# Kernel tuning notes

Measured on AMD Instinct MI355X. Metric: run time of the kernel, lower is better.

## Reference

```python
import jax, jax.numpy as jnp
import numpy as np
from jax import lax


def _l2norm(x):
    return x / jnp.sqrt(jnp.sum(x * x, axis=-1, keepdims=True) + 1e-6)


def setup_inputs() -> dict:
    key = jax.random.key(0)
    kq, kk, kv, kb = jax.random.split(key, 4)
    b, h, L, d = 2, 8, 4096, 128
    return {
        "q": jax.random.normal(kq, (b, h, L, d), dtype=jnp.float32),
        "k": jax.random.normal(kk, (b, h, L, d), dtype=jnp.float32),
        "v": jax.random.normal(kv, (b, h, L, d), dtype=jnp.float32),
        "beta": jax.random.uniform(kb, (b, h, L), dtype=jnp.float32),
        "chunk_size": 32,
    }


def reference(q, k, v, beta, chunk_size):
    # Chunk-wise Delta-rule linear attention (faithful to delta_rule_chunkwise).
    b, h, L, dk = q.shape
    dv = v.shape[-1]
    c = int(chunk_size)
    pad = (-L) % c
    if pad:
        q = jnp.pad(q, ((0, 0), (0, 0), (0, pad), (0, 0)))
        k = jnp.pad(k, ((0, 0), (0, 0), (0, pad), (0, 0)))
        v = jnp.pad(v, ((0, 0), (0, 0), (0, pad), (0, 0)))
        beta = jnp.pad(beta, ((0, 0), (0, 0), (0, pad)))
    Lp = L + pad
    n = Lp // c

    q = _l2norm(q)
    k = _l2norm(k)
    v = v * beta[..., None]
    k_beta = k * beta[..., None]

    # [b, h, n, c, d]
    qc = q.reshape(b, h, n, c, dk)
    kc = k.reshape(b, h, n, c, dk)
    vc = v.reshape(b, h, n, c, dv)
    kbc = k_beta.reshape(b, h, n, c, dk)

    tri_incl = jnp.triu(jnp.ones((c, c), dtype=bool), 0)   # diag + upper
    tri_strict = jnp.triu(jnp.ones((c, c), dtype=bool), 1)  # strictly upper

    # Strictly-lower negated Gram matrix, then sequential forward substitution
    # building rows of (I - T)^{-1} (matches the in-place torch loop exactly).
    attn = -(kbc @ jnp.swapaxes(kc, -1, -2))
    attn = jnp.where(tri_incl, 0.0, attn)
    for i in range(1, c):
        row = attn[..., i, :]                                  # [b,h,n,c]
        row = row + jnp.einsum('bhnj,bhnjc->bhnc', row, attn)  # only cols < i change
        attn = attn.at[..., i, :].set(row)
    attn = attn + jnp.eye(c, dtype=attn.dtype)

    u = attn @ vc    # [b,h,n,c,dv]
    w = attn @ kbc   # [b,h,n,c,dk]

    # Inter-chunk recurrence over n chunks.
    def step(S, inp):
        q_i, k_i, u_i, w_i = inp            # [b,h,c,d]
        attn_local = q_i @ jnp.swapaxes(k_i, -1, -2)
        attn_local = jnp.where(tri_strict, 0.0, attn_local)
        u_i = u_i - w_i @ S
        o_i = q_i @ S + attn_local @ u_i
        S = S + jnp.swapaxes(k_i, -1, -2) @ u_i
        return S, o_i

    S0 = jnp.zeros((b, h, dk, dv), dtype=q.dtype)
    xs = (jnp.moveaxis(qc, 2, 0), jnp.moveaxis(kc, 2, 0),
          jnp.moveaxis(u, 2, 0), jnp.moveaxis(w, 2, 0))
    S, o = lax.scan(step, S0, xs)
    o = jnp.moveaxis(o, 0, 2).reshape(b, h, Lp, dv)[:, :, :L]
    return o, S
```

## Files before the change

### kernel.cpp

```cpp
#include <hip/hip_runtime.h>
#include <math.h>

typedef unsigned short u16;
typedef __attribute__((ext_vector_type(8))) short s8v;
typedef __attribute__((ext_vector_type(4))) float f4v;

#define BH 16
#define SEQ 4096
#define DD 128

__device__ __forceinline__ float b2f(u16 h){ union{unsigned u; float f;} v; v.u=((unsigned)h)<<16; return v.f; }
__device__ __forceinline__ u16 f2b(float f){ union{float f; unsigned u;} v; v.f=f; unsigned r=v.u+0x7FFFu+((v.u>>16)&1u); return (u16)(r>>16); }
__device__ __forceinline__ f4v mm16(s8v a, s8v b, f4v c){ return __builtin_amdgcn_mfma_f32_16x16x32_bf16(a,b,c,0,0,0); }
__device__ __forceinline__ float dot4(float4 a, float4 b){ return a.x*b.x+a.y*b.y+a.z*b.z+a.w*b.w; }

__global__ __launch_bounds__(512,4) void p1_kernel(
    const float* __restrict__ gq, const float* __restrict__ gk,
    const float* __restrict__ gv, const float* __restrict__ gbeta,
    u16* __restrict__ gw, u16* __restrict__ gqen, u16* __restrict__ gu0,
    u16* __restrict__ gknT, float* __restrict__ gik, float* __restrict__ gout)
{
  __shared__ u16 qnh[32][136], qnl[32][136];
  __shared__ u16 arena1[10240];
  __shared__ u16 vbT[128][40], kbT[128][40];
  __shared__ u16 arena2[8704];
  __shared__ float Amat[32][33];
  __shared__ float bet[32];

  u16 (*knh)[136] = (u16(*)[136])arena1;
  u16 (*knl)[136] = (u16(*)[136])(arena1+4352);
  u16 (*wTT)[40]  = (u16(*)[40])arena1;
  u16 (*u0T)[40]  = (u16(*)[40])(arena1+5120);
  u16 (*vb16)[136]= (u16(*)[136])arena2;
  u16 (*kb16)[136]= (u16(*)[136])(arena2+4352);
  u16 (*Tb)[40]   = (u16(*)[40])arena2;
  u16 (*ALb)[40]  = (u16(*)[40])(arena2+1280);

  const int cid = blockIdx.x, bh = cid>>7, ci = cid&127;
  const int t = threadIdx.x, wave = t>>6, lane = t&63, m = lane&15, qq = lane>>4;
  const size_t tokbase = (size_t)bh*SEQ + (size_t)ci*32;
  const size_t base = tokbase*DD;

  for (int p=0;p<2;++p){
    int idx = t + (p<<9);
    int r = idx>>5, c4 = (idx&31)<<2;
    float4 qv = *(const float4*)(gq + base + r*DD + c4);
    float4 kv = *(const float4*)(gk + base + r*DD + c4);
    float4 vv = *(const float4*)(gv + base + r*DD + c4);
    float nq = dot4(qv,qv), nk = dot4(kv,kv);
    nq += __shfl_xor(nq,1); nq += __shfl_xor(nq,2); nq += __shfl_xor(nq,4);
    nq += __shfl_xor(nq,8); nq += __shfl_xor(nq,16);
    nk += __shfl_xor(nk,1); nk += __shfl_xor(nk,2); nk += __shfl_xor(nk,4);
    nk += __shfl_xor(nk,8); nk += __shfl_xor(nk,16);
    float iq = 1.f/sqrtf(nq+1e-6f), ik = 1.f/sqrtf(nk+1e-6f);
    float bb = gbeta[tokbase + r];
    if ((idx&31)==0){ gik[tokbase+r]=ik; bet[r]=bb; }
    float qa[4]={qv.x,qv.y,qv.z,qv.w}, ka[4]={kv.x,kv.y,kv.z,kv.w}, va[4]={vv.x,vv.y,vv.z,vv.w};
    union{u16 s[4]; uint2 v;} hq,lq,hk,lk,sv,sb;
    #pragma unroll
    for(int i=0;i<4;++i){
      float qn = qa[i]*iq; u16 h1=f2b(qn); hq.s[i]=h1; lq.s[i]=f2b(qn-b2f(h1));
      float kn = ka[i]*ik; u16 h2=f2b(kn); hk.s[i]=h2; lk.s[i]=f2b(kn-b2f(h2));
      sv.s[i]=f2b(va[i]*bb); sb.s[i]=f2b(kn*bb);
    }
    *(uint2*)&qnh[r][c4]=hq.v; *(uint2*)&qnl[r][c4]=lq.v;
    *(uint2*)&knh[r][c4]=hk.v; *(uint2*)&knl[r][c4]=lk.v;
    *(uint2*)&vb16[r][c4]=sv.v; *(uint2*)&kb16[r][c4]=sb.v;
  }
  __syncthreads();

  {
    u16* kdst = gknT + ((size_t)(bh*32 + (ci>>2)))*16384 + (size_t)((ci&3)*32);
    for (int g=0; g<2; ++g){
      int tau = t + (g<<9);
      int r = tau & 31, d0 = (tau>>5)<<2;
      union{u16 s[4]; uint2 v;} vv, kk, kn4;
      vv.v  = *(uint2*)&vb16[r][d0];
      kk.v  = *(uint2*)&kb16[r][d0];
      kn4.v = *(uint2*)&knh[r][d0];
      #pragma unroll
      for(int i=0;i<4;++i){
        vbT[d0+i][r] = vv.s[i];
        kbT[d0+i][r] = kk.s[i];
        kdst[(size_t)(d0+i)*128 + r] = kn4.s[i];
      }
    }
  }
  __syncthreads();

  {
    const int TI[3]={0,1,1}, TJ[3]={0,0,1};
    if (wave < 3){
      int ti=TI[wave], tj=TJ[wave];
      f4v acc = {0.f,0.f,0.f,0.f};
      #pragma unroll
      for(int kc=0;kc<4;++kc){
        int ko = kc*32 + qq*8;
        s8v ah = *(const s8v*)&knh[ti*16+m][ko];
        s8v al = *(const s8v*)&knl[ti*16+m][ko];
        s8v bhv = *(const s8v*)&knh[tj*16+m][ko];
        s8v blv = *(const s8v*)&knl[tj*16+m][ko];
        acc = mm16(ah,bhv,acc); acc = mm16(ah,blv,acc); acc = mm16(al,bhv,acc);
      }
      #pragma unroll
      for(int r=0;r<4;++r){
        int row = ti*16+qq*4+r, col = tj*16+m;
        Amat[row][col] = (col<row)? (-bet[row]*acc[r]) : 0.f;
      }
    } else if (wave < 6){
      int ti=TI[wave-3], tj=TJ[wave-3];
      f4v acc = {0.f,0.f,0.f,0.f};
      #pragma unroll
      for(int kc=0;kc<4;++kc){
        int ko = kc*32 + qq*8;
        s8v ah = *(const s8v*)&qnh[ti*16+m][ko];
        s8v al = *(const s8v*)&qnl[ti*16+m][ko];
        s8v bhv = *(const s8v*)&knh[tj*16+m][ko];
        s8v blv = *(const s8v*)&knl[tj*16+m][ko];
        acc = mm16(ah,bhv,acc); acc = mm16(ah,blv,acc); acc = mm16(al,bhv,acc);
      }
      #pragma unroll
      for(int r=0;r<4;++r){
        int row = ti*16+qq*4+r, col = tj*16+m;
        ALb[row][col] = (col<=row)? f2b(acc[r]) : (u16)0;
      }
    } else if (wave == 6){
      #pragma unroll
      for(int r=0;r<4;++r) ALb[qq*4+r][16+m] = (u16)0;
    }
  }
  __syncthreads();

  if (t < 32){
    float a[32];
    #pragma unroll
    for(int i=0;i<32;++i) a[i] = (t<i)? Amat[i][t] : 0.f;
    #pragma unroll
    for(int i=2;i<32;++i){
      float s = a[i];
      #pragma unroll
      for(int j=1;j<i;++j) s += __shfl(a[i],j)*a[j];
      a[i] = s;
    }
    #pragma unroll
    for(int i=0;i<32;++i) Tb[i][t] = f2b(a[i] + (i==t?1.f:0.f));
  }
  __syncthreads();

  #pragma unroll
  for (int q8 = 0; q8 < 4; ++q8){
    int tau = wave + q8*8;
    bool isu = (tau < 16);
    int tile16 = tau & 15, rt = tile16>>3, dt = tile16&7;
    s8v aT = *(const s8v*)&Tb[rt*16+m][qq*8];
    s8v bB = isu ? *(const s8v*)&vbT[dt*16+m][qq*8] : *(const s8v*)&kbT[dt*16+m][qq*8];
    f4v acc = {0.f,0.f,0.f,0.f};
    acc = mm16(aT,bB,acc);
    int tok0 = rt*16 + qq*4, dcol = dt*16+m;
    u16* gdst = isu ? gu0 : gw;
    u16 (*ldst)[40] = isu ? u0T : wTT;
    union{u16 s[4]; uint2 v;} pk;
    #pragma unroll
    for(int r=0;r<4;++r){
      u16 hv = f2b(acc[r]); pk.s[r]=hv;
      gdst[(tokbase + tok0 + r)*DD + dcol] = hv;
    }
    *(uint2*)&ldst[dcol][tok0] = pk.v;
  }
  __syncthreads();

  #pragma unroll
  for (int q8 = 0; q8 < 4; ++q8){
    int tau = wave + q8*8;
    bool isq = (tau < 16);
    int tile16 = tau & 15, rt = tile16>>3, dt = tile16&7;
    s8v aA = *(const s8v*)&ALb[rt*16+m][qq*8];
    s8v bB = isq ? *(const s8v*)&wTT[dt*16+m][qq*8] : *(const s8v*)&u0T[dt*16+m][qq*8];
    f4v acc = {0.f,0.f,0.f,0.f};
    acc = mm16(aA,bB,acc);
    int tok0 = rt*16+qq*4, dcol = dt*16+m;
    #pragma unroll
    for(int r=0;r<4;++r){
      size_t gi = (tokbase+tok0+r)*DD + dcol;
      if (isq){
        float qn = b2f(qnh[tok0+r][dcol]) + b2f(qnl[tok0+r][dcol]);
        gqen[gi] = f2b(acc[r] - qn);
      } else {
        gout[gi] = acc[r];
      }
    }
  }
}

template<int C>
__global__ __launch_bounds__(256) void merge_kernel(
    const float* __restrict__ gk, const float* __restrict__ gik,
    u16* __restrict__ gw, u16* __restrict__ gqen, u16* __restrict__ gu0,
    float* __restrict__ gout)
{
  constexpr int P = 2048 / C;
  constexpr int SM = C + 8;
  __shared__ u16 k1[C][136];
  __shared__ u16 w1T[128][SM], u01T[128][SM];
  __shared__ u16 Mw[C][SM], MG[C][SM];
  const int bh = blockIdx.x / P, pr = blockIdx.x % P;
  const int t = threadIdx.x, wave = t>>6, lane = t&63, m = lane&15, qq = lane>>4;
  const int base1 = pr*2*C, base2 = base1 + C;
  const size_t tb1 = (size_t)bh*SEQ + base1, tb2 = (size_t)bh*SEQ + base2;

  for(int p=0;p<C*32/256;++p){
    int idx = t + (p<<8); int j = idx>>5, c4 = (idx&31)<<2;
    float ik = gik[tb1 + j];
    float4 kv = *(const float4*)(gk + (tb1+j)*DD + c4);
    union{u16 s[4]; uint2 v;} pk;
    pk.s[0]=f2b(kv.x*ik); pk.s[1]=f2b(kv.y*ik); pk.s[2]=f2b(kv.z*ik); pk.s[3]=f2b(kv.w*ik);
    *(uint2*)&k1[j][c4] = pk.v;
  }
  for(int p=0;p<C*16/256;++p){
    int idx = t + (p<<8); int j = idx>>4, d8 = (idx&15)<<3;
    s8v wv = *(const s8v*)(gw + (tb1+j)*DD + d8);
    s8v uv = *(const s8v*)(gu0 + (tb1+j)*DD + d8);
    const u16* wsp = (const u16*)&wv; const u16* usp = (const u16*)&uv;
    for(int i=0;i<8;++i){ w1T[d8+i][j]=wsp[i]; u01T[d8+i][j]=usp[i]; }
  }
  __syncthreads();

  constexpr int NT = (C/16)*(C/16);
  for(int tile = wave; tile < NT; tile += 4){
    int ti = tile/(C/16), tj = tile%(C/16);
    f4v aw = {0.f,0.f,0.f,0.f}, ag = {0.f,0.f,0.f,0.f};
    for(int kc=0;kc<4;++kc){
      int ko = kc*32 + qq*8;
      s8v b  = *(const s8v*)&k1[tj*16+m][ko];
      s8v a1 = *(const s8v*)(gw   + (tb2 + ti*16+m)*DD + ko);
      s8v a2 = *(const s8v*)(gqen + (tb2 + ti*16+m)*DD + ko);
      aw = mm16(a1,b,aw); ag = mm16(a2,b,ag);
    }
    for(int r=0;r<4;++r){
      Mw[ti*16+qq*4+r][tj*16+m] = f2b(aw[r]);
      MG[ti*16+qq*4+r][tj*16+m] = f2b(ag[r]);
    }
  }
  __syncthreads();

  {
    const u16 (*Ma)[SM] = (wave==0||wave==2) ? Mw : MG;
    const u16 (*Bt)[SM] = (wave<2) ? w1T : u01T;
    for(int tile=0; tile<(C/16)*8; ++tile){
      int ti = tile>>3, dt = tile&7;
      f4v acc = {0.f,0.f,0.f,0.f};
      for(int kc=0;kc<C/32;++kc){
        int ko = kc*32+qq*8;
        s8v a = *(const s8v*)&Ma[ti*16+m][ko];
        s8v b = *(const s8v*)&Bt[dt*16+m][ko];
        acc = mm16(a,b,acc);
      }
      int d = dt*16+m;
      for(int r=0;r<4;++r){
        size_t gi = (tb2 + ti*16 + qq*4 + r)*DD + d;
        if (wave==0)      gw[gi]   = f2b(b2f(gw[gi])   - acc[r]);
        else if (wave==1) gqen[gi] = f2b(b2f(gqen[gi]) - acc[r]);
        else if (wave==2) gu0[gi]  = f2b(b2f(gu0[gi])  - acc[r]);
        else              gout[gi] = gout[gi] - acc[r];
      }
    }
  }
}

__global__ __launch_bounds__(512) void p2_kernel(
    const u16* __restrict__ gw, const u16* __restrict__ gqen,
    const u16* __restrict__ gu0, const u16* __restrict__ knT,
    float* __restrict__ gout)
{
  __shared__ u16 lSb[2][16][136];
  __shared__ u16 lub[2][16][136];
  const int bh = blockIdx.x & 15, slice = blockIdx.x >> 4;
  const int t = threadIdx.x, wave = t>>6, lane = t&63, m = lane&15, qq = lane>>4;
  f4v S = {0.f,0.f,0.f,0.f};
  float* out_o = gout;
  float* out_S = gout + (size_t)BH*SEQ*DD;
  const size_t bhb = (size_t)bh*SEQ;

  for (int ci = 0; ci < 32; ++ci) {
    {
      int d0 = wave*16 + qq*4;
      for(int r=0;r<4;++r){
        float v = S[r]; u16 hi = f2b(v); u16 lo = f2b(v - b2f(hi));
        lSb[0][m][d0+r] = hi; lSb[1][m][d0+r] = lo;
      }
    }
    __syncthreads();
    const u16* wbase = gw   + (bhb + (size_t)ci*128)*DD;
    const u16* qbase = gqen + (bhb + (size_t)ci*128)*DD;
    f4v au = {0.f,0.f,0.f,0.f}, ao = {0.f,0.f,0.f,0.f};
    for (int kc = 0; kc < 4; ++kc) {
      int ko = kc*32 + qq*8;
      s8v bhv = *(const s8v*)&lSb[0][m][ko];
      s8v blv = *(const s8v*)&lSb[1][m][ko];
      s8v awv = *(const s8v*)(wbase + (size_t)(wave*16 + m)*DD + ko);
      s8v aqv = *(const s8v*)(qbase + (size_t)(wave*16 + m)*DD + ko);
      au = mm16(awv,bhv,au); au = mm16(awv,blv,au);
      ao = mm16(aqv,bhv,ao); ao = mm16(aqv,blv,ao);
    }
    {
      int tokb = ci*128 + wave*16 + qq*4;
      int dv = slice*16 + m;
      for(int r=0;r<4;++r){
        size_t gi = (bhb + tokb + r)*DD + dv;
        float uv = b2f(gu0[gi]) - au[r];
        u16 hi = f2b(uv); u16 lo = f2b(uv - b2f(hi));
        int j = wave*16 + qq*4 + r;
        lub[0][m][j] = hi; lub[1][m][j] = lo;
        out_o[gi] = out_o[gi] - ao[r];
      }
    }
    __syncthreads();
    const u16* ktb = knT + ((size_t)(bh*32 + ci))*16384;
    for (int jc = 0; jc < 4; ++jc) {
      int ko = jc*32 + qq*8;
      s8v a   = *(const s8v*)(ktb + (size_t)(wave*16 + m)*DD + ko);
      s8v bhv = *(const s8v*)&lub[0][m][ko];
      s8v blv = *(const s8v*)&lub[1][m][ko];
      S = mm16(a,bhv,S); S = mm16(a,blv,S);
    }
  }
  {
    int d0 = wave*16 + qq*4, dv = slice*16 + m;
    for(int r=0;r<4;++r)
      out_S[(size_t)bh*16384 + (size_t)(d0+r)*DD + dv] = S[r];
  }
}

extern "C" void kernel_launch(void* const* d_in, const int* in_sizes, int n_in,
                              void* d_out, int out_size, void* d_ws, size_t ws_size,
                              hipStream_t stream) {
  const float* q    = (const float*)d_in[0];
  const float* k    = (const float*)d_in[1];
  const float* v    = (const float*)d_in[2];
  const float* beta = (const float*)d_in[3];
  u16* wsu  = (u16*)d_ws;
  u16* gw   = wsu;
  u16* gqen = wsu + 8388608;
  u16* gu0  = wsu + 16777216;
  u16* knT  = wsu + 25165824;
  float* gik = (float*)(wsu + 33554432);
  float* out = (float*)d_out;

  p1_kernel<<<dim3(2048), dim3(512), 0, stream>>>(q, k, v, beta, gw, gqen, gu0, knT, gik, out);
  merge_kernel<32><<<dim3(1024), dim3(256), 0, stream>>>(k, gik, gw, gqen, gu0, out);
  merge_kernel<64><<<dim3(512),  dim3(256), 0, stream>>>(k, gik, gw, gqen, gu0, out);
  p2_kernel<<<dim3(128), dim3(512), 0, stream>>>(gw, gqen, gu0, knT, out);
}
```

Before: 396.9 us.

## Prefetch next chunk's operands into registers in the sequential scan kernel

The inter-chunk recurrence kernel now loads the next chunk's w, q, kT fragments, u0 values and partial outputs into registers during the current iteration, so global-memory latency overlaps with the MFMA work instead of sitting on the serial dependency chain. __syncthreads is replaced by a custom barrier that waits only on LDS counters (lgkmcnt), which lets the outstanding global prefetch loads stay in flight across the barrier. Register pressure rises from the doubled fragment buffers, and the last iteration issues a redundant wrap-around prefetch.

```diff
diff --git a/kernel.cpp b/kernel.cpp
--- a/kernel.cpp
+++ b/kernel.cpp
@@ -13,6 +13,9 @@
 __device__ __forceinline__ u16 f2b(float f){ union{float f; unsigned u;} v; v.f=f; unsigned r=v.u+0x7FFFu+((v.u>>16)&1u); return (u16)(r>>16); }
 __device__ __forceinline__ f4v mm16(s8v a, s8v b, f4v c){ return __builtin_amdgcn_mfma_f32_16x16x32_bf16(a,b,c,0,0,0); }
 __device__ __forceinline__ float dot4(float4 a, float4 b){ return a.x*b.x+a.y*b.y+a.z*b.z+a.w*b.w; }
+__device__ __forceinline__ void bar_lds(){
+  asm volatile("s_waitcnt lgkmcnt(0)\n\ts_barrier" ::: "memory");
+}
 
 __global__ __launch_bounds__(512,4) void p1_kernel(
     const float* __restrict__ gq, const float* __restrict__ gk,
@@ -280,52 +283,95 @@
   float* out_o = gout;
   float* out_S = gout + (size_t)BH*SEQ*DD;
   const size_t bhb = (size_t)bh*SEQ;
+  const int dv = slice*16 + m;
+
+  s8v wf[4], qf[4], kf[4];
+  float u0f[4], pf[4];
+  {
+    const u16* wbase = gw   + bhb*DD + (size_t)(wave*16+m)*DD;
+    const u16* qbase = gqen + bhb*DD + (size_t)(wave*16+m)*DD;
+    const u16* ktb   = knT + ((size_t)(bh*32))*16384 + (size_t)(wave*16+m)*DD;
+    #pragma unroll
+    for(int kc=0;kc<4;++kc){
+      wf[kc] = *(const s8v*)(wbase + kc*32 + qq*8);
+      qf[kc] = *(const s8v*)(qbase + kc*32 + qq*8);
+      kf[kc] = *(const s8v*)(ktb   + kc*32 + qq*8);
+    }
+    #pragma unroll
+    for(int r=0;r<4;++r){
+      size_t gi = (bhb + wave*16 + qq*4 + r)*DD + dv;
+      u0f[r] = b2f(gu0[gi]);
+      pf[r]  = out_o[gi];
+    }
+  }
 
   for (int ci = 0; ci < 32; ++ci) {
+    s8v wn[4], qn4[4], kn4[4];
+    float u0n[4], pn[4];
+    {
+      int cn = (ci + 1) & 31;
+      const u16* wbase = gw   + (bhb + (size_t)cn*128)*DD + (size_t)(wave*16+m)*DD;
+      const u16* qbase = gqen + (bhb + (size_t)cn*128)*DD + (size_t)(wave*16+m)*DD;
+      const u16* ktb   = knT + ((size_t)(bh*32+cn))*16384 + (size_t)(wave*16+m)*DD;
+      #pragma unroll
+      for(int kc=0;kc<4;++kc){
+        wn[kc]  = *(const s8v*)(wbase + kc*32 + qq*8);
+        qn4[kc] = *(const s8v*)(qbase + kc*32 + qq*8);
+        kn4[kc] = *(const s8v*)(ktb   + kc*32 + qq*8);
+      }
+      #pragma unroll
+      for(int r=0;r<4;++r){
+        size_t gi = (bhb + (size_t)cn*128 + wave*16 + qq*4 + r)*DD + dv;
+        u0n[r] = b2f(gu0[gi]);
+        pn[r]  = out_o[gi];
+      }
+    }
+
     {
       int d0 = wave*16 + qq*4;
+      #pragma unroll
       for(int r=0;r<4;++r){
         float v = S[r]; u16 hi = f2b(v); u16 lo = f2b(v - b2f(hi));
         lSb[0][m][d0+r] = hi; lSb[1][m][d0+r] = lo;
       }
     }
-    __syncthreads();
-    const u16* wbase = gw   + (bhb + (size_t)ci*128)*DD;
-    const u16* qbase = gqen + (bhb + (size_t)ci*128)*DD;
+    bar_lds();
     f4v au = {0.f,0.f,0.f,0.f}, ao = {0.f,0.f,0.f,0.f};
+    #pragma unroll
     for (int kc = 0; kc < 4; ++kc) {
       int ko = kc*32 + qq*8;
       s8v bhv = *(const s8v*)&lSb[0][m][ko];
       s8v blv = *(const s8v*)&lSb[1][m][ko];
-      s8v awv = *(const s8v*)(wbase + (size_t)(wave*16 + m)*DD + ko);
-      s8v aqv = *(const s8v*)(qbase + (size_t)(wave*16 + m)*DD + ko);
-      au = mm16(awv,bhv,au); au = mm16(awv,blv,au);
-      ao = mm16(aqv,bhv,ao); ao = mm16(aqv,blv,ao);
+      au = mm16(wf[kc],bhv,au); au = mm16(wf[kc],blv,au);
+      ao = mm16(qf[kc],bhv,ao); ao = mm16(qf[kc],blv,ao);
     }
     {
-      int tokb = ci*128 + wave*16 + qq*4;
-      int dv = slice*16 + m;
-      for(int r=0;r<4;++r){
-        size_t gi = (bhb + tokb + r)*DD + dv;
-        float uv = b2f(gu0[gi]) - au[r];
+      int j0 = wave*16 + qq*4;
+      #pragma unroll
+      for(int r=0;r<4;++r){
+        size_t gi = (bhb + (size_t)ci*128 + j0 + r)*DD + dv;
+        float uv = u0f[r] - au[r];
         u16 hi = f2b(uv); u16 lo = f2b(uv - b2f(hi));
-        int j = wave*16 + qq*4 + r;
-        lub[0][m][j] = hi; lub[1][m][j] = lo;
-        out_o[gi] = out_o[gi] - ao[r];
-      }
-    }
-    __syncthreads();
-    const u16* ktb = knT + ((size_t)(bh*32 + ci))*16384;
+        lub[0][m][j0+r] = hi; lub[1][m][j0+r] = lo;
+        out_o[gi] = pf[r] - ao[r];
+      }
+    }
+    bar_lds();
+    #pragma unroll
     for (int jc = 0; jc < 4; ++jc) {
       int ko = jc*32 + qq*8;
-      s8v a   = *(const s8v*)(ktb + (size_t)(wave*16 + m)*DD + ko);
       s8v bhv = *(const s8v*)&lub[0][m][ko];
       s8v blv = *(const s8v*)&lub[1][m][ko];
-      S = mm16(a,bhv,S); S = mm16(a,blv,S);
-    }
-  }
-  {
-    int d0 = wave*16 + qq*4, dv = slice*16 + m;
+      S = mm16(kf[jc],bhv,S); S = mm16(kf[jc],blv,S);
+    }
+    #pragma unroll
+    for(int kc=0;kc<4;++kc){ wf[kc]=wn[kc]; qf[kc]=qn4[kc]; kf[kc]=kn4[kc]; }
+    #pragma unroll
+    for(int r=0;r<4;++r){ u0f[r]=u0n[r]; pf[r]=pn[r]; }
+  }
+  {
+    int d0 = wave*16 + qq*4;
+    #pragma unroll
     for(int r=0;r<4;++r)
       out_S[(size_t)bh*16384 + (size_t)(d0+r)*DD + dv] = S[r];
   }
```

New measurement: 371.3 us. -6.5%, faster.
